# Kernel optimization log

Measured on AMD Instinct MI355X. Metric: run time of the kernel, lower is better.

The kernel has to match this reference:

```python
import jax, jax.numpy as jnp
import numpy as np

B, T, D, H, C = 2048, 512, 5, 128, 10  # batch, seq_len, input_dim, hidden_dim, num_classes


def setup_inputs() -> dict:
    key = jax.random.key(0)
    ks = jax.random.split(key, 13)
    s = 1.0 / np.sqrt(H)  # PyTorch LSTM init range

    def u(k, shape):
        return jax.random.uniform(k, shape, jnp.float32, -s, s)

    return {
        "x": jax.random.normal(ks[0], (B, T, D), jnp.float32),
        # layer 0 (gate order i,f,g,o as in PyTorch)
        "w_ih0": u(ks[1], (4 * H, D)),
        "w_hh0": u(ks[2], (4 * H, H)),
        "b_ih0": u(ks[3], (4 * H,)),
        "b_hh0": u(ks[4], (4 * H,)),
        # layer 1
        "w_ih1": u(ks[5], (4 * H, H)),
        "w_hh1": u(ks[6], (4 * H, H)),
        "b_ih1": u(ks[7], (4 * H,)),
        "b_hh1": u(ks[8], (4 * H,)),
        # classifier: Linear(H, H//2) -> ReLU -> Linear(H//2, C); dropout inactive (eval)
        "cw1": u(ks[9], (H // 2, H)),
        "cb1": u(ks[10], (H // 2,)),
        "cw2": u(ks[11], (C, H // 2)),
        "cb2": u(ks[12], (C,)),
    }


def _lstm_layer(xs, w_ih, w_hh, b_ih, b_hh):
    # xs: [T, B, in]; returns (ys [T, B, H], h_T [B, H])
    Hh = w_hh.shape[1]
    b = b_ih + b_hh

    def step(carry, x_t):
        h, c = carry
        gates = x_t @ w_ih.T + h @ w_hh.T + b  # [B, 4H]
        i, f, g, o = jnp.split(gates, 4, axis=-1)
        c = jax.nn.sigmoid(f) * c + jax.nn.sigmoid(i) * jnp.tanh(g)
        h = jax.nn.sigmoid(o) * jnp.tanh(c)
        return (h, c), h

    Bn = xs.shape[1]
    h0 = jnp.zeros((Bn, Hh), xs.dtype)
    (h_T, _), ys = jax.lax.scan(step, (h0, h0), xs)
    return ys, h_T


def reference(x, w_ih0, w_hh0, b_ih0, b_hh0, w_ih1, w_hh1, b_ih1, b_hh1, cw1, cb1, cw2, cb2):
    xs = jnp.transpose(x, (1, 0, 2))  # [T, B, D]
    ys0, _ = _lstm_layer(xs, w_ih0, w_hh0, b_ih0, b_hh0)
    # inter-layer dropout(0.2) is a no-op in eval mode
    _, last_hidden = _lstm_layer(ys0, w_ih1, w_hh1, b_ih1, b_hh1)  # h_n[-1]: [B, H]
    # classifier (Dropout(0.3) inactive in eval)
    r = jax.nn.relu(last_hidden @ cw1.T + cb1)
    output = r @ cw2.T + cb2  # [B, C]
    return (output, last_hidden)
```

## Files before the change

### kernel.cpp

```cpp
#include <hip/hip_runtime.h>

typedef unsigned short ushort;
typedef unsigned int uint;
typedef __bf16 bf16_t;
typedef bf16_t bf16x8 __attribute__((ext_vector_type(8)));
typedef float f32x4 __attribute__((ext_vector_type(4)));

#define B_ 2048
#define T_ 512
#define D_ 5
#define H_ 128
#define C_ 10
#define BT 16
#define BLK 512
#define NP 128
#define CH 8
#define H0STR 168
#define H1STR 136

static __device__ __forceinline__ float b2f(ushort u) {
    return __builtin_bit_cast(float, ((uint)u) << 16);
}
static __device__ __forceinline__ ushort f2b(float f) {
    uint u = __builtin_bit_cast(uint, f);
    u += 0x7FFFu + ((u >> 16) & 1u);
    return (ushort)(u >> 16);
}
static __device__ __forceinline__ float sigf(float x) {
    return __builtin_amdgcn_rcpf(1.0f + __expf(-x));
}
static __device__ __forceinline__ float tanhf_(float x) {
    return 1.0f - 2.0f * __builtin_amdgcn_rcpf(1.0f + __expf(2.0f * x));
}
static __device__ __forceinline__ float ldf(const void* p, long i, bool m32) {
    return m32 ? ((const float*)p)[i] : b2f(((const ushort*)p)[i]);
}
static __device__ __forceinline__ bf16x8 ld16(const ushort* p) {
    return __builtin_bit_cast(bf16x8, *(const uint4*)p);
}
static __device__ __forceinline__ bf16x8 ldfrag(const void* p, long idx, bool m32) {
    if (!m32) return ld16((const ushort*)p + idx);
    const float* f = (const float*)p + idx;
    union { ushort u[8]; bf16x8 v; } r;
#pragma unroll
    for (int j = 0; j < 8; ++j) r.u[j] = f2b(f[j]);
    return r.v;
}
static __device__ __forceinline__ f32x4 splat4(float v) {
    f32x4 r = {v, v, v, v};
    return r;
}

__global__ void detect_dtype(const ushort* __restrict__ w, int* __restrict__ flag) {
    __shared__ int cnt;
    if (threadIdx.x == 0) cnt = 0;
    __syncthreads();
    int local = 0;
    for (int i = threadIdx.x; i < 16384; i += 256)
        if ((uint)(w[i] & 0x7F80u) >= 0x4180u) ++local;
    atomicAdd(&cnt, local);
    __syncthreads();
    if (threadIdx.x == 0) *flag = (cnt > 512) ? 1 : 0;
}

__global__ void init_flags(int* __restrict__ prog) {
    prog[threadIdx.x] = 0;
}

__global__ __launch_bounds__(BLK, 2) void lstm2_pipe(
    const void* __restrict__ x,
    const void* __restrict__ wih0, const void* __restrict__ whh0,
    const void* __restrict__ bih0, const void* __restrict__ bhh0,
    const void* __restrict__ wih1, const void* __restrict__ whh1,
    const void* __restrict__ bih1, const void* __restrict__ bhh1,
    const void* __restrict__ cw1, const void* __restrict__ cb1,
    const void* __restrict__ cw2, const void* __restrict__ cb2,
    const int* __restrict__ flag,
    ushort* __restrict__ fifo, int* __restrict__ prog_p, int* __restrict__ prog_c,
    int F, void* __restrict__ out)
{
    __shared__ __align__(16) ushort sA[2][BT * H0STR];
    __shared__ __align__(16) ushort sB[2][BT * H1STR];
    __shared__ float rs[BT * 64];

    const bool m32 = (*flag) != 0;
    const int tid  = threadIdx.x;
    const int w    = tid >> 6;
    const int lane = tid & 63;
    const int quad = lane >> 4;
    const int l16  = lane & 15;

    if ((int)blockIdx.x < NP) {
        const int p   = blockIdx.x;
        const int bt0 = p * BT;
        ushort* myfifo = fifo + (long)p * F * (BT * H_);

        for (int i = tid; i < BT * 32; i += BLK) {
            int row = i >> 5, cc = i & 31;
            ushort v0 = (cc < 5) ? f2b(ldf(x, ((long)(bt0 + row) * T_) * D_ + cc, m32))
                                 : (ushort)0;
            sA[0][row * H0STR + 128 + cc] = v0;
            sA[1][row * H0STR + 128 + cc] = 0;
        }

        bf16x8 wh0c[4][4];
        bf16x8 xbf[4];
        float  b0v[4];
#pragma unroll
        for (int g = 0; g < 4; ++g) {
            const int n = g * 128 + w * 16 + l16;
#pragma unroll
            for (int kt = 0; kt < 4; ++kt)
                wh0c[g][kt] = ldfrag(whh0, (long)n * 128 + kt * 32 + quad * 8, m32);
            union { ushort u[8]; bf16x8 v; } xt;
#pragma unroll
            for (int j = 0; j < 8; ++j) xt.u[j] = 0;
            if (quad == 0) {
#pragma unroll
                for (int j = 0; j < 5; ++j) xt.u[j] = f2b(ldf(wih0, (long)n * D_ + j, m32));
            }
            xbf[g] = xt.v;
            b0v[g] = ldf(bih0, n, m32) + ldf(bhh0, n, m32);
        }
        __syncthreads();

        bf16x8 h0f[4];
        {
            uint4 z = make_uint4(0, 0, 0, 0);
            h0f[0] = h0f[1] = h0f[2] = h0f[3] = __builtin_bit_cast(bf16x8, z);
        }
        f32x4 c0 = splat4(0.f);
        const int xr = tid / 5, xc = tid - (tid / 5) * 5;

#pragma unroll 1
        for (int t = 0; t < T_; ++t) {
            const int rb = t & 1, wb = (t + 1) & 1;
            if ((t & (CH - 1)) == 0 && t > 0) {
                if (tid == 0) {
                    __hip_atomic_store(&prog_p[p], t, __ATOMIC_RELEASE,
                                       __HIP_MEMORY_SCOPE_AGENT);
                    int need = t + CH - F;
                    if (need > 0)
                        while (__hip_atomic_load(&prog_c[p], __ATOMIC_ACQUIRE,
                                                 __HIP_MEMORY_SCOPE_AGENT) < need)
                            __builtin_amdgcn_s_sleep(2);
                }
                __syncthreads();
            }
            float xv = 0.f;
            const bool stage = (tid < 80) && (t < T_ - 1);
            if (stage) xv = ldf(x, ((long)(bt0 + xr) * T_ + (t + 1)) * D_ + xc, m32);

            f32x4 a[4];
#pragma unroll
            for (int g = 0; g < 4; ++g) a[g] = splat4(b0v[g]);
#pragma unroll
            for (int kt = 0; kt < 4; ++kt)
#pragma unroll
                for (int g = 0; g < 4; ++g)
                    a[g] = __builtin_amdgcn_mfma_f32_16x16x32_bf16(
                        h0f[kt], wh0c[g][kt], a[g], 0, 0, 0);
            {
                bf16x8 ha4 = ld16(&sA[rb][l16 * H0STR + 128 + quad * 8]);
#pragma unroll
                for (int g = 0; g < 4; ++g)
                    a[g] = __builtin_amdgcn_mfma_f32_16x16x32_bf16(
                        ha4, xbf[g], a[g], 0, 0, 0);
            }
            ushort* fs = myfifo + (long)(t & (F - 1)) * (BT * H_);
#pragma unroll
            for (int r = 0; r < 4; ++r) {
                float iv = sigf(a[0][r]), fv = sigf(a[1][r]);
                float gv = tanhf_(a[2][r]), ov = sigf(a[3][r]);
                float cv = fv * c0[r] + iv * gv;
                c0[r] = cv;
                ushort hv = f2b(ov * tanhf_(cv));
                int row = quad * 4 + r;
                sA[wb][row * H0STR + w * 16 + l16] = hv;
                fs[row * H_ + w * 16 + l16] = hv;
            }
            if (stage) sA[wb][xr * H0STR + 128 + xc] = f2b(xv);
            __syncthreads();
#pragma unroll
            for (int kt = 0; kt < 4; ++kt)
                h0f[kt] = ld16(&sA[wb][l16 * H0STR + kt * 32 + quad * 8]);
        }
        if (tid == 0)
            __hip_atomic_store(&prog_p[p], T_, __ATOMIC_RELEASE,
                               __HIP_MEMORY_SCOPE_AGENT);
    } else {
        const int p   = blockIdx.x - NP;
        const int bt0 = p * BT;
        const ushort* myfifo = fifo + (long)p * F * (BT * H_);

        for (int i = tid; i < BT * H_; i += BLK) {
            int row = i >> 7, cc = i & 127;
            sB[0][row * H1STR + cc] = 0;
        }

        bf16x8 wi1f[4][4], wh1f[4][4];
        float  b1v[4];
#pragma unroll
        for (int g = 0; g < 4; ++g) {
            const int n = g * 128 + w * 16 + l16;
#pragma unroll
            for (int kt = 0; kt < 4; ++kt) {
                wi1f[g][kt] = ldfrag(wih1, (long)n * 128 + kt * 32 + quad * 8, m32);
                wh1f[g][kt] = ldfrag(wih1 == whh1 ? whh1 : whh1,
                                     (long)n * 128 + kt * 32 + quad * 8, m32);
            }
            b1v[g] = ldf(bih1, n, m32) + ldf(bhh1, n, m32);
        }

        if (tid == 0) {
            while (__hip_atomic_load(&prog_p[p], __ATOMIC_ACQUIRE,
                                     __HIP_MEMORY_SCOPE_AGENT) < 2 * CH)
                __builtin_amdgcn_s_sleep(2);
        }
        __syncthreads();
        {
            int row = tid >> 5, col4 = (tid & 31) * 4;
            uint2 d = *(const uint2*)(myfifo + tid * 4);
            *(uint2*)&sA[0][row * H0STR + col4] = d;
        }
        __syncthreads();

        f32x4 c1 = splat4(0.f);

#pragma unroll 1
        for (int t = 0; t < T_; ++t) {
            const int rb = t & 1, wb = (t + 1) & 1;
            if (((t + 1) & (CH - 1)) == 0 && t + 1 < T_) {
                if (tid == 0) {
                    int target = t + 1 + CH;
                    if (target > T_) target = T_;
                    while (__hip_atomic_load(&prog_p[p], __ATOMIC_ACQUIRE,
                                             __HIP_MEMORY_SCOPE_AGENT) < target)
                        __builtin_amdgcn_s_sleep(2);
                    __hip_atomic_store(&prog_c[p], t + 1, __ATOMIC_RELEASE,
                                       __HIP_MEMORY_SCOPE_AGENT);
                }
                __syncthreads();
            }
            uint2 pf = make_uint2(0, 0);
            const bool hn = (t + 1 < T_);
            if (hn) pf = *(const uint2*)(myfifo
                          + (long)((t + 1) & (F - 1)) * (BT * H_) + tid * 4);

            f32x4 a[4];
#pragma unroll
            for (int g = 0; g < 4; ++g) a[g] = splat4(b1v[g]);
#pragma unroll
            for (int kt = 0; kt < 4; ++kt) {
                bf16x8 h0a = ld16(&sA[rb][l16 * H0STR + kt * 32 + quad * 8]);
#pragma unroll
                for (int g = 0; g < 4; ++g)
                    a[g] = __builtin_amdgcn_mfma_f32_16x16x32_bf16(
                        h0a, wi1f[g][kt], a[g], 0, 0, 0);
            }
#pragma unroll
            for (int kt = 0; kt < 4; ++kt) {
                bf16x8 hb = ld16(&sB[rb][l16 * H1STR + kt * 32 + quad * 8]);
#pragma unroll
                for (int g = 0; g < 4; ++g)
                    a[g] = __builtin_amdgcn_mfma_f32_16x16x32_bf16(
                        hb, wh1f[g][kt], a[g], 0, 0, 0);
            }
#pragma unroll
            for (int r = 0; r < 4; ++r) {
                float iv = sigf(a[0][r]), fv = sigf(a[1][r]);
                float gv = tanhf_(a[2][r]), ov = sigf(a[3][r]);
                float cv = fv * c1[r] + iv * gv;
                c1[r] = cv;
                sB[wb][(quad * 4 + r) * H1STR + w * 16 + l16] = f2b(ov * tanhf_(cv));
            }
            if (hn) {
                int row = tid >> 5, col4 = (tid & 31) * 4;
                *(uint2*)&sA[wb][row * H0STR + col4] = pf;
            }
            __syncthreads();
        }

        if (tid < 256) {
            int m = tid >> 4, j0 = (tid & 15) * 4;
            float s0 = ldf(cb1, j0, m32), s1 = ldf(cb1, j0 + 1, m32);
            float s2 = ldf(cb1, j0 + 2, m32), s3 = ldf(cb1, j0 + 3, m32);
            const ushort* hr = &sB[0][m * H1STR];
#pragma unroll 4
            for (int k = 0; k < 128; ++k) {
                float hv = b2f(hr[k]);
                s0 += hv * ldf(cw1, (long)j0 * 128 + k, m32);
                s1 += hv * ldf(cw1, (long)(j0 + 1) * 128 + k, m32);
                s2 += hv * ldf(cw1, (long)(j0 + 2) * 128 + k, m32);
                s3 += hv * ldf(cw1, (long)(j0 + 3) * 128 + k, m32);
            }
            rs[m * 64 + j0]     = fmaxf(s0, 0.f);
            rs[m * 64 + j0 + 1] = fmaxf(s1, 0.f);
            rs[m * 64 + j0 + 2] = fmaxf(s2, 0.f);
            rs[m * 64 + j0 + 3] = fmaxf(s3, 0.f);
        }
        __syncthreads();
        if (tid < 160) {
            int m = tid / 10, cc = tid - m * 10;
            float s = ldf(cb2, cc, m32);
#pragma unroll
            for (int j = 0; j < 64; ++j)
                s += rs[m * 64 + j] * ldf(cw2, (long)cc * 64 + j, m32);
            long oi = (long)(bt0 + m) * C_ + cc;
            if (m32) ((float*)out)[oi] = s; else ((ushort*)out)[oi] = f2b(s);
        }
        for (int idx = tid; idx < BT * H_; idx += BLK) {
            int m = idx >> 7, k = idx & 127;
            float v = b2f(sB[0][m * H1STR + k]);
            long oi = (long)B_ * C_ + (long)(bt0 + m) * H_ + k;
            if (m32) ((float*)out)[oi] = v; else ((ushort*)out)[oi] = f2b(v);
        }
    }
}

__global__ __launch_bounds__(BLK, 2) void lstm2_mono(
    const void* __restrict__ x,
    const void* __restrict__ wih0, const void* __restrict__ whh0,
    const void* __restrict__ bih0, const void* __restrict__ bhh0,
    const void* __restrict__ wih1, const void* __restrict__ whh1,
    const void* __restrict__ bih1, const void* __restrict__ bhh1,
    const void* __restrict__ cw1, const void* __restrict__ cb1,
    const void* __restrict__ cw2, const void* __restrict__ cb2,
    const int* __restrict__ flag, void* __restrict__ out)
{
    __shared__ __align__(16) ushort h0s[2][BT * H0STR];
    __shared__ __align__(16) ushort h1s[2][BT * H1STR];
    __shared__ float rs[BT * 64];
    __shared__ uint4 xstash[4 * 8 * 64];

    const bool m32 = (*flag) != 0;
    const int tid  = threadIdx.x;
    const int w    = tid >> 6;
    const int lane = tid & 63;
    const int quad = lane >> 4;
    const int l16  = lane & 15;
    const int bt0  = blockIdx.x * BT;

    for (int i = tid; i < BT * 32; i += BLK) {
        int row = i >> 5, cc = i & 31;
        ushort v0 = (cc < 5) ? f2b(ldf(x, ((long)(bt0 + row) * T_) * D_ + cc, m32)) : (ushort)0;
        h0s[0][row * H0STR + 128 + cc] = v0;
        h0s[1][row * H0STR + 128 + cc] = 0;
    }
    for (int i = tid; i < BT * H_; i += BLK) {
        int row = i >> 7, cc = i & 127;
        h1s[1][row * H1STR + cc] = 0;
    }

    bf16x8 wh0c[4][4], wi1f[4][4], wh1f[4][4];
    float  b0v[4], b1v[4];
#pragma unroll
    for (int g = 0; g < 4; ++g) {
        const int n = g * 128 + w * 16 + l16;
#pragma unroll
        for (int kt = 0; kt < 4; ++kt) {
            wh0c[g][kt] = ldfrag(whh0, (long)n * 128 + kt * 32 + quad * 8, m32);
            wi1f[g][kt] = ldfrag(wih1, (long)n * 128 + kt * 32 + quad * 8, m32);
            wh1f[g][kt] = ldfrag(whh1, (long)n * 128 + kt * 32 + quad * 8, m32);
        }
        union { ushort u[8]; uint4 q; } xt;
        xt.q = make_uint4(0, 0, 0, 0);
        if (quad == 0) {
#pragma unroll
            for (int j = 0; j < 5; ++j) xt.u[j] = f2b(ldf(wih0, (long)n * D_ + j, m32));
        }
        xstash[(g * 8 + w) * 64 + lane] = xt.q;
        b0v[g] = ldf(bih0, n, m32) + ldf(bhh0, n, m32);
        b1v[g] = ldf(bih1, n, m32) + ldf(bhh1, n, m32);
    }
    __syncthreads();

    bf16x8 h0f[4];
    {
        uint4 z = make_uint4(0, 0, 0, 0);
        h0f[0] = h0f[1] = h0f[2] = h0f[3] = __builtin_bit_cast(bf16x8, z);
    }
    f32x4 c0 = splat4(0.f), c1 = splat4(0.f);
    const int xr = tid / 5, xc = tid - (tid / 5) * 5;

#pragma unroll 1
    for (int t = 0; t < T_; ++t) {
        const int wb = (t + 1) & 1, rb = t & 1;
        float xv = 0.f;
        const bool stage = (tid < 80) && (t < T_ - 1);
        if (stage) xv = ldf(x, ((long)(bt0 + xr) * T_ + (t + 1)) * D_ + xc, m32);

        f32x4 a[4];
#pragma unroll
        for (int g = 0; g < 4; ++g) a[g] = splat4(b0v[g]);
#pragma unroll
        for (int kt = 0; kt < 4; ++kt)
#pragma unroll
            for (int g = 0; g < 4; ++g)
                a[g] = __builtin_amdgcn_mfma_f32_16x16x32_bf16(
                    h0f[kt], wh0c[g][kt], a[g], 0, 0, 0);
        {
            bf16x8 ha4 = ld16(&h0s[rb][l16 * H0STR + 128 + quad * 8]);
#pragma unroll
            for (int g = 0; g < 4; ++g) {
                bf16x8 xb = __builtin_bit_cast(bf16x8, xstash[(g * 8 + w) * 64 + lane]);
                a[g] = __builtin_amdgcn_mfma_f32_16x16x32_bf16(ha4, xb, a[g], 0, 0, 0);
            }
        }
        ushort h0w[4];
#pragma unroll
        for (int r = 0; r < 4; ++r) {
            float iv = sigf(a[0][r]), fv = sigf(a[1][r]);
            float gv = tanhf_(a[2][r]), ov = sigf(a[3][r]);
            float cv = fv * c0[r] + iv * gv;
            c0[r] = cv;
            h0w[r] = f2b(ov * tanhf_(cv));
        }
#pragma unroll
        for (int r = 0; r < 4; ++r)
            h0s[wb][(quad * 4 + r) * H0STR + w * 16 + l16] = h0w[r];
        if (stage) h0s[wb][xr * H0STR + 128 + xc] = f2b(xv);
        __syncthreads();
#pragma unroll
        for (int kt = 0; kt < 4; ++kt)
            h0f[kt] = ld16(&h0s[wb][l16 * H0STR + kt * 32 + quad * 8]);

#pragma unroll
        for (int g = 0; g < 4; ++g) a[g] = splat4(b1v[g]);
#pragma unroll
        for (int kt = 0; kt < 4; ++kt)
#pragma unroll
            for (int g = 0; g < 4; ++g)
                a[g] = __builtin_amdgcn_mfma_f32_16x16x32_bf16(
                    h0f[kt], wi1f[g][kt], a[g], 0, 0, 0);
#pragma unroll
        for (int kt = 0; kt < 4; ++kt) {
            bf16x8 hb = ld16(&h1s[wb][l16 * H1STR + kt * 32 + quad * 8]);
#pragma unroll
            for (int g = 0; g < 4; ++g)
                a[g] = __builtin_amdgcn_mfma_f32_16x16x32_bf16(
                    hb, wh1f[g][kt], a[g], 0, 0, 0);
        }
#pragma unroll
        for (int r = 0; r < 4; ++r) {
            float iv = sigf(a[0][r]), fv = sigf(a[1][r]);
            float gv = tanhf_(a[2][r]), ov = sigf(a[3][r]);
            float cv = fv * c1[r] + iv * gv;
            c1[r] = cv;
            h1s[wb ^ 1][(quad * 4 + r) * H1STR + w * 16 + l16] = f2b(ov * tanhf_(cv));
        }
    }
    __syncthreads();

    if (tid < 256) {
        int m = tid >> 4, j0 = (tid & 15) * 4;
        float s0 = ldf(cb1, j0, m32), s1 = ldf(cb1, j0 + 1, m32);
        float s2 = ldf(cb1, j0 + 2, m32), s3 = ldf(cb1, j0 + 3, m32);
        const ushort* hr = &h1s[1][m * H1STR];
#pragma unroll 4
        for (int k = 0; k < 128; ++k) {
            float hv = b2f(hr[k]);
            s0 += hv * ldf(cw1, (long)j0 * 128 + k, m32);
            s1 += hv * ldf(cw1, (long)(j0 + 1) * 128 + k, m32);
            s2 += hv * ldf(cw1, (long)(j0 + 2) * 128 + k, m32);
            s3 += hv * ldf(cw1, (long)(j0 + 3) * 128 + k, m32);
        }
        rs[m * 64 + j0]     = fmaxf(s0, 0.f);
        rs[m * 64 + j0 + 1] = fmaxf(s1, 0.f);
        rs[m * 64 + j0 + 2] = fmaxf(s2, 0.f);
        rs[m * 64 + j0 + 3] = fmaxf(s3, 0.f);
    }
    __syncthreads();
    if (tid < 160) {
        int m = tid / 10, cc = tid - m * 10;
        float s = ldf(cb2, cc, m32);
#pragma unroll
        for (int j = 0; j < 64; ++j) s += rs[m * 64 + j] * ldf(cw2, (long)cc * 64 + j, m32);
        long oi = (long)(bt0 + m) * C_ + cc;
        if (m32) ((float*)out)[oi] = s; else ((ushort*)out)[oi] = f2b(s);
    }
    for (int idx = tid; idx < BT * H_; idx += BLK) {
        int m = idx >> 7, k = idx & 127;
        float v = b2f(h1s[1][m * H1STR + k]);
        long oi = (long)B_ * C_ + (long)(bt0 + m) * H_ + k;
        if (m32) ((float*)out)[oi] = v; else ((ushort*)out)[oi] = f2b(v);
    }
}

extern "C" void kernel_launch(void* const* d_in, const int* in_sizes, int n_in,
                              void* d_out, int out_size, void* d_ws, size_t ws_size,
                              hipStream_t stream) {
    (void)in_sizes; (void)n_in; (void)out_size;
    int* prog  = (int*)d_ws;
    int* flag  = (int*)((char*)d_ws + 4096);
    ushort* fifo = (ushort*)((char*)d_ws + 8192);

    hipLaunchKernelGGL(detect_dtype, dim3(1), dim3(256), 0, stream,
                       (const ushort*)d_in[2], flag);

    const size_t slot = (size_t)NP * BT * H_ * sizeof(ushort);
    int F = 0;
    if (ws_size >= 8192 + 64 * slot) F = 64;
    else if (ws_size >= 8192 + 32 * slot) F = 32;

    if (F) {
        hipLaunchKernelGGL(init_flags, dim3(1), dim3(256), 0, stream, prog);
        hipLaunchKernelGGL(lstm2_pipe, dim3(2 * NP), dim3(BLK), 0, stream,
                           d_in[0], d_in[1], d_in[2], d_in[3], d_in[4],
                           d_in[5], d_in[6], d_in[7], d_in[8],
                           d_in[9], d_in[10], d_in[11], d_in[12],
                           (const int*)flag, fifo, prog, prog + NP, F, d_out);
    } else {
        hipLaunchKernelGGL(lstm2_mono, dim3(B_ / BT), dim3(BLK), 0, stream,
                           d_in[0], d_in[1], d_in[2], d_in[3], d_in[4],
                           d_in[5], d_in[6], d_in[7], d_in[8],
                           d_in[9], d_in[10], d_in[11], d_in[12],
                           (const int*)flag, d_out);
    }
}
```

Before: 908.6 us.

## Batch x prefetch per chunk, swizzle LDS layout, lighten barriers and atomics

The layer-0 producer no longer loads one x element per timestep. It now stages an 8-step chunk of x into a dedicated LDS buffer and prefetches the next chunk into registers, which takes a global load off every step's critical path. The hidden-state LDS buffers switch to an XOR-swizzled 136-stride layout so the MFMA fragment reads hit fewer bank conflicts. Per-step __syncthreads is replaced with a bare lgkmcnt wait plus s_barrier, and the spin-waits use relaxed loads followed by one acquire fence. The trade is more complex indexing, extra LDS, and tighter memory-ordering assumptions around the global FIFO writes.

```diff
diff --git a/kernel.cpp b/kernel.cpp
--- a/kernel.cpp
+++ b/kernel.cpp
@@ -17,6 +17,8 @@
 #define CH 8
 #define H0STR 168
 #define H1STR 136
+#define SSTR 136
+#define XSTR 40
 
 static __device__ __forceinline__ float b2f(ushort u) {
     return __builtin_bit_cast(float, ((uint)u) << 16);
@@ -49,6 +51,14 @@
 static __device__ __forceinline__ f32x4 splat4(float v) {
     f32x4 r = {v, v, v, v};
     return r;
+}
+static __device__ __forceinline__ int swz(int row, int col) {
+    return row * SSTR + ((((col >> 4) ^ (row >> 3)) << 4) | (col & 15));
+}
+static __device__ __forceinline__ void bar_lds() {
+    asm volatile("s_waitcnt lgkmcnt(0)" ::: "memory");
+    __builtin_amdgcn_s_barrier();
+    asm volatile("" ::: "memory");
 }
 
 __global__ void detect_dtype(const ushort* __restrict__ w, int* __restrict__ flag) {
@@ -79,8 +89,9 @@
     ushort* __restrict__ fifo, int* __restrict__ prog_p, int* __restrict__ prog_c,
     int F, void* __restrict__ out)
 {
-    __shared__ __align__(16) ushort sA[2][BT * H0STR];
-    __shared__ __align__(16) ushort sB[2][BT * H1STR];
+    __shared__ __align__(16) ushort sA[2][BT * SSTR];
+    __shared__ __align__(16) ushort sB[2][BT * SSTR];
+    __shared__ __align__(16) ushort xch[CH * 16 * XSTR];
     __shared__ float rs[BT * 64];
 
     const bool m32 = (*flag) != 0;
@@ -95,13 +106,19 @@
         const int bt0 = p * BT;
         ushort* myfifo = fifo + (long)p * F * (BT * H_);
 
-        for (int i = tid; i < BT * 32; i += BLK) {
-            int row = i >> 5, cc = i & 31;
-            ushort v0 = (cc < 5) ? f2b(ldf(x, ((long)(bt0 + row) * T_) * D_ + cc, m32))
-                                 : (ushort)0;
-            sA[0][row * H0STR + 128 + cc] = v0;
-            sA[1][row * H0STR + 128 + cc] = 0;
-        }
+        const int e0 = tid;
+        const int r0 = e0 / 40, rem0 = e0 - r0 * 40;
+        const int tt0 = rem0 / 5, d0 = rem0 - tt0 * 5;
+        const long xo0 = (long)(bt0 + r0) * T_ * D_ + (long)tt0 * D_ + d0;
+        const int xdst0 = (tt0 * 16 + r0) * XSTR + d0;
+        const int e1 = tid + 512;
+        const int r1 = e1 / 40, rem1 = e1 - r1 * 40;
+        const int tt1 = rem1 / 5, d1 = rem1 - tt1 * 5;
+        const long xo1 = (long)(bt0 + r1) * T_ * D_ + (long)tt1 * D_ + d1;
+        const int xdst1 = (tt1 * 16 + r1) * XSTR + d1;
+        const bool has1 = (tid < 128);
+
+        for (int i = tid; i < CH * 16 * XSTR; i += BLK) xch[i] = 0;
 
         bf16x8 wh0c[4][4];
         bf16x8 xbf[4];
@@ -122,6 +139,16 @@
             xbf[g] = xt.v;
             b0v[g] = ldf(bih0, n, m32) + ldf(bhh0, n, m32);
         }
+        __syncthreads();
+
+        {
+            float v0 = ldf(x, xo0, m32);
+            float v1 = has1 ? ldf(x, xo1, m32) : 0.f;
+            xch[xdst0] = f2b(v0);
+            if (has1) xch[xdst1] = f2b(v1);
+        }
+        float xp0 = ldf(x, xo0 + (long)(CH * D_), m32);
+        float xp1 = has1 ? ldf(x, xo1 + (long)(CH * D_), m32) : 0.f;
         __syncthreads();
 
         bf16x8 h0f[4];
@@ -130,26 +157,28 @@
             h0f[0] = h0f[1] = h0f[2] = h0f[3] = __builtin_bit_cast(bf16x8, z);
         }
         f32x4 c0 = splat4(0.f);
-        const int xr = tid / 5, xc = tid - (tid / 5) * 5;
 
 #pragma unroll 1
         for (int t = 0; t < T_; ++t) {
-            const int rb = t & 1, wb = (t + 1) & 1;
+            const int wb = (t + 1) & 1;
             if ((t & (CH - 1)) == 0 && t > 0) {
+                __syncthreads();
+                xch[xdst0] = f2b(xp0);
+                if (has1) xch[xdst1] = f2b(xp1);
                 if (tid == 0) {
                     __hip_atomic_store(&prog_p[p], t, __ATOMIC_RELEASE,
                                        __HIP_MEMORY_SCOPE_AGENT);
                     int need = t + CH - F;
                     if (need > 0)
-                        while (__hip_atomic_load(&prog_c[p], __ATOMIC_ACQUIRE,
+                        while (__hip_atomic_load(&prog_c[p], __ATOMIC_RELAXED,
                                                  __HIP_MEMORY_SCOPE_AGENT) < need)
                             __builtin_amdgcn_s_sleep(2);
                 }
                 __syncthreads();
-            }
-            float xv = 0.f;
-            const bool stage = (tid < 80) && (t < T_ - 1);
-            if (stage) xv = ldf(x, ((long)(bt0 + xr) * T_ + (t + 1)) * D_ + xc, m32);
+                const int tb = t + CH;
+                xp0 = (tb + tt0 < T_) ? ldf(x, xo0 + (long)tb * D_, m32) : 0.f;
+                xp1 = (has1 && tb + tt1 < T_) ? ldf(x, xo1 + (long)tb * D_, m32) : 0.f;
+            }
 
             f32x4 a[4];
 #pragma unroll
@@ -161,7 +190,7 @@
                     a[g] = __builtin_amdgcn_mfma_f32_16x16x32_bf16(
                         h0f[kt], wh0c[g][kt], a[g], 0, 0, 0);
             {
-                bf16x8 ha4 = ld16(&sA[rb][l16 * H0STR + 128 + quad * 8]);
+                bf16x8 ha4 = ld16(&xch[((t & (CH - 1)) * 16 + l16) * XSTR + quad * 8]);
 #pragma unroll
                 for (int g = 0; g < 4; ++g)
                     a[g] = __builtin_amdgcn_mfma_f32_16x16x32_bf16(
@@ -176,15 +205,15 @@
                 c0[r] = cv;
                 ushort hv = f2b(ov * tanhf_(cv));
                 int row = quad * 4 + r;
-                sA[wb][row * H0STR + w * 16 + l16] = hv;
+                sA[wb][swz(row, w * 16 + l16)] = hv;
                 fs[row * H_ + w * 16 + l16] = hv;
             }
-            if (stage) sA[wb][xr * H0STR + 128 + xc] = f2b(xv);
-            __syncthreads();
+            bar_lds();
 #pragma unroll
             for (int kt = 0; kt < 4; ++kt)
-                h0f[kt] = ld16(&sA[wb][l16 * H0STR + kt * 32 + quad * 8]);
-        }
+                h0f[kt] = ld16(&sA[wb][swz(l16, kt * 32 + quad * 8)]);
+        }
+        __syncthreads();
         if (tid == 0)
             __hip_atomic_store(&prog_p[p], T_, __ATOMIC_RELEASE,
                                __HIP_MEMORY_SCOPE_AGENT);
@@ -193,10 +222,7 @@
         const int bt0 = p * BT;
         const ushort* myfifo = fifo + (long)p * F * (BT * H_);
 
-        for (int i = tid; i < BT * H_; i += BLK) {
-            int row = i >> 7, cc = i & 127;
-            sB[0][row * H1STR + cc] = 0;
-        }
+        for (int i = tid; i < BT * SSTR; i += BLK) sB[0][i] = 0;
 
         bf16x8 wi1f[4][4], wh1f[4][4];
         float  b1v[4];
@@ -206,22 +232,22 @@
 #pragma unroll
             for (int kt = 0; kt < 4; ++kt) {
                 wi1f[g][kt] = ldfrag(wih1, (long)n * 128 + kt * 32 + quad * 8, m32);
-                wh1f[g][kt] = ldfrag(wih1 == whh1 ? whh1 : whh1,
-                                     (long)n * 128 + kt * 32 + quad * 8, m32);
+                wh1f[g][kt] = ldfrag(whh1, (long)n * 128 + kt * 32 + quad * 8, m32);
             }
             b1v[g] = ldf(bih1, n, m32) + ldf(bhh1, n, m32);
         }
 
         if (tid == 0) {
-            while (__hip_atomic_load(&prog_p[p], __ATOMIC_ACQUIRE,
+            while (__hip_atomic_load(&prog_p[p], __ATOMIC_RELAXED,
                                      __HIP_MEMORY_SCOPE_AGENT) < 2 * CH)
                 __builtin_amdgcn_s_sleep(2);
+            __builtin_amdgcn_fence(__ATOMIC_ACQUIRE, "agent");
         }
         __syncthreads();
         {
             int row = tid >> 5, col4 = (tid & 31) * 4;
             uint2 d = *(const uint2*)(myfifo + tid * 4);
-            *(uint2*)&sA[0][row * H0STR + col4] = d;
+            *(uint2*)&sA[0][swz(row, col4)] = d;
         }
         __syncthreads();
 
@@ -234,9 +260,10 @@
                 if (tid == 0) {
                     int target = t + 1 + CH;
                     if (target > T_) target = T_;
-                    while (__hip_atomic_load(&prog_p[p], __ATOMIC_ACQUIRE,
+                    while (__hip_atomic_load(&prog_p[p], __ATOMIC_RELAXED,
                                              __HIP_MEMORY_SCOPE_AGENT) < target)
                         __builtin_amdgcn_s_sleep(2);
+                    __builtin_amdgcn_fence(__ATOMIC_ACQUIRE, "agent");
                     __hip_atomic_store(&prog_c[p], t + 1, __ATOMIC_RELEASE,
                                        __HIP_MEMORY_SCOPE_AGENT);
                 }
@@ -252,7 +279,7 @@
             for (int g = 0; g < 4; ++g) a[g] = splat4(b1v[g]);
 #pragma unroll
             for (int kt = 0; kt < 4; ++kt) {
-                bf16x8 h0a = ld16(&sA[rb][l16 * H0STR + kt * 32 + quad * 8]);
+                bf16x8 h0a = ld16(&sA[rb][swz(l16, kt * 32 + quad * 8)]);
 #pragma unroll
                 for (int g = 0; g < 4; ++g)
                     a[g] = __builtin_amdgcn_mfma_f32_16x16x32_bf16(
@@ -260,7 +287,7 @@
             }
 #pragma unroll
             for (int kt = 0; kt < 4; ++kt) {
-                bf16x8 hb = ld16(&sB[rb][l16 * H1STR + kt * 32 + quad * 8]);
+                bf16x8 hb = ld16(&sB[rb][swz(l16, kt * 32 + quad * 8)]);
 #pragma unroll
                 for (int g = 0; g < 4; ++g)
                     a[g] = __builtin_amdgcn_mfma_f32_16x16x32_bf16(
@@ -272,27 +299,32 @@
                 float gv = tanhf_(a[2][r]), ov = sigf(a[3][r]);
                 float cv = fv * c1[r] + iv * gv;
                 c1[r] = cv;
-                sB[wb][(quad * 4 + r) * H1STR + w * 16 + l16] = f2b(ov * tanhf_(cv));
+                sB[wb][swz(quad * 4 + r, w * 16 + l16)] = f2b(ov * tanhf_(cv));
             }
             if (hn) {
                 int row = tid >> 5, col4 = (tid & 31) * 4;
-                *(uint2*)&sA[wb][row * H0STR + col4] = pf;
-            }
-            __syncthreads();
+                *(uint2*)&sA[wb][swz(row, col4)] = pf;
+            }
+            bar_lds();
         }
 
         if (tid < 256) {
             int m = tid >> 4, j0 = (tid & 15) * 4;
             float s0 = ldf(cb1, j0, m32), s1 = ldf(cb1, j0 + 1, m32);
             float s2 = ldf(cb1, j0 + 2, m32), s3 = ldf(cb1, j0 + 3, m32);
-            const ushort* hr = &sB[0][m * H1STR];
-#pragma unroll 4
-            for (int k = 0; k < 128; ++k) {
-                float hv = b2f(hr[k]);
-                s0 += hv * ldf(cw1, (long)j0 * 128 + k, m32);
-                s1 += hv * ldf(cw1, (long)(j0 + 1) * 128 + k, m32);
-                s2 += hv * ldf(cw1, (long)(j0 + 2) * 128 + k, m32);
-                s3 += hv * ldf(cw1, (long)(j0 + 3) * 128 + k, m32);
+            const int mswz = m >> 3;
+#pragma unroll
+            for (int kb = 0; kb < 8; ++kb) {
+                const ushort* hp = &sB[0][m * SSTR + ((kb ^ mswz) << 4)];
+#pragma unroll
+                for (int kk = 0; kk < 16; ++kk) {
+                    int k = kb * 16 + kk;
+                    float hv = b2f(hp[kk]);
+                    s0 += hv * ldf(cw1, (long)j0 * 128 + k, m32);
+                    s1 += hv * ldf(cw1, (long)(j0 + 1) * 128 + k, m32);
+                    s2 += hv * ldf(cw1, (long)(j0 + 2) * 128 + k, m32);
+                    s3 += hv * ldf(cw1, (long)(j0 + 3) * 128 + k, m32);
+                }
             }
             rs[m * 64 + j0]     = fmaxf(s0, 0.f);
             rs[m * 64 + j0 + 1] = fmaxf(s1, 0.f);
@@ -311,7 +343,7 @@
         }
         for (int idx = tid; idx < BT * H_; idx += BLK) {
             int m = idx >> 7, k = idx & 127;
-            float v = b2f(sB[0][m * H1STR + k]);
+            float v = b2f(sB[0][swz(m, k)]);
             long oi = (long)B_ * C_ + (long)(bt0 + m) * H_ + k;
             if (m32) ((float*)out)[oi] = v; else ((ushort*)out)[oi] = f2b(v);
         }
```

After: 929.9 us. 1.02x slower.
